# Kernel optimization log

Measured on AMD Instinct MI355X. Metric: run time of the kernel, lower is better.

## Reference

```python
import jax, jax.numpy as jnp
import numpy as np
from jax import lax
from jax.scipy.special import logsumexp

NUM_BINS = 1001          # num_bins
K = 127                  # num_quantized_bins = 2**(8-1) - 1 (signed int8, non-narrow)
HALF = NUM_BINS // 2     # 500
EPS = 1e-4               # smoothing_eps
NEG = -1e30              # mask value for logsumexp


def setup_inputs() -> dict:
    key = jax.random.key(0)
    x = jax.random.normal(key, (8, 4096, 1024), dtype=jnp.float32)
    return {"x": x}


def _smooth_logits(v, valid, L):
    # Faithful to smooth_normalize_distribution: hist += eps*is_zeros - eps1*n_nonzeros
    is_zero = valid & (v == 0)
    n_zeros = jnp.sum(is_zero).astype(jnp.float32)
    n_nz = L.astype(jnp.float32) - n_zeros
    eps1 = EPS * n_zeros / jnp.maximum(n_nz, 1.0)
    logits = v + EPS * is_zero.astype(jnp.float32) - eps1 * n_nz
    return logits, n_nz


def reference(x):
    absmax = jnp.max(jnp.abs(x))
    edges = jnp.linspace(-absmax, absmax, NUM_BINS + 1)           # hist_edges, len 1002
    counts, _ = jnp.histogram(x.ravel(), bins=edges)
    hist = lax.stop_gradient(counts.astype(jnp.float32))          # torch.histc(...).int()
    csum = jnp.concatenate([jnp.zeros(1, jnp.float32), jnp.cumsum(hist)])  # exclusive prefix
    total = csum[-1]
    hist_pad = jnp.concatenate([hist, jnp.zeros(NUM_BINS, jnp.float32)])
    k = jnp.arange(NUM_BINS)

    def per_candidate(i):
        start = HALF - i
        stop = HALF + i + 1
        L = 2 * i + 1                          # length of sliced histogram
        valid = k < L
        sliced = lax.dynamic_slice(hist_pad, (start,), (NUM_BINS,))  # first L entries valid
        left = csum[start]                     # sum(hist[:start])
        right = total - csum[stop]             # sum(hist[stop:])
        p = sliced.at[0].add(left).at[L - 1].add(right)
        m = L // K                             # num_merged_bins
        seg = jnp.minimum(k // m, K - 1)       # merged-bin id per position (remainder -> last)
        seg_v = jnp.where(valid, seg, K)       # dump invalid into extra segment
        qb = jax.ops.segment_sum(jnp.where(valid, sliced, 0.0), seg_v, num_segments=K + 1)[:K]
        nz = valid & (sliced != 0)
        # norm for bin j counts nonzeros in its range; last bin uses stop=-1 (excludes k=L-1)
        cnt_mask = nz & (k != L - 1)
        norms = jax.ops.segment_sum(cnt_mask.astype(jnp.float32), seg_v, num_segments=K + 1)[:K]
        nk = norms[seg]
        qbk = qb[seg]
        # q[start:stop] = qb[j]/norm where norm != 0; k=L-1 never assigned; q[sliced==0]=0
        q = jnp.where(nz & (k != L - 1) & (nk > 0), qbk / jnp.maximum(nk, 1.0), 0.0)

        p_log, _ = _smooth_logits(p, valid, L)
        q_log, n_nz_q = _smooth_logits(q, valid, L)
        lZp = logsumexp(jnp.where(valid, p_log, NEG))
        lZq = logsumexp(jnp.where(valid, q_log, NEG))
        lp = p_log - lZp
        lq = q_log - lZq
        probs = jnp.where(valid, jnp.exp(lp), 0.0)
        kl = jnp.sum(probs * (lp - lq) * valid)
        kl = jnp.where(n_nz_q > 0, kl, jnp.inf)  # q all-zero -> divergence = inf
        return edges[stop], kl

    ivals = jnp.arange(K // 2, HALF + 1)        # i = 63 .. 500 (438 candidates)
    thresholds, divergence = jax.vmap(per_candidate)(ivals)
    return thresholds[jnp.argmin(divergence)]
```

## Files before the change

kernel.cpp:

```cpp
#include <hip/hip_runtime.h>
#include <math.h>

#define NBINS 1001
#define KQ 127
#define HALFB 500
#define SEPS 1e-4f
#define NCAND 438
#define IMIN 63


static __device__ __forceinline__ float edge_at(int j, float stepv, float negabs) {
    return __fadd_rn(__fmul_rn((float)j, stepv), negabs);
}

static __device__ __forceinline__ void blockSum2(double& a, double& b, double* s8) {
    for (int s = 32; s > 0; s >>= 1) {
        a += __shfl_down(a, s, 64);
        b += __shfl_down(b, s, 64);
    }
    const int w = threadIdx.x >> 6, l = threadIdx.x & 63;
    __syncthreads();
    if (l == 0) { s8[w] = a; s8[4 + w] = b; }
    __syncthreads();
    a = (s8[0] + s8[1]) + (s8[2] + s8[3]);
    b = (s8[4] + s8[5]) + (s8[6] + s8[7]);
}

static __device__ __forceinline__ double blockSum1(double a, double* s8) {
    for (int s = 32; s > 0; s >>= 1) a += __shfl_down(a, s, 64);
    const int w = threadIdx.x >> 6, l = threadIdx.x & 63;
    __syncthreads();
    if (l == 0) s8[w] = a;
    __syncthreads();
    return (s8[0] + s8[1]) + (s8[2] + s8[3]);
}

static __device__ __forceinline__ void blockMax2(float& a, float& b, double* s8) {
    for (int s = 32; s > 0; s >>= 1) {
        a = fmaxf(a, __shfl_down(a, s, 64));
        b = fmaxf(b, __shfl_down(b, s, 64));
    }
    const int w = threadIdx.x >> 6, l = threadIdx.x & 63;
    __syncthreads();
    if (l == 0) { s8[w] = (double)a; s8[4 + w] = (double)b; }
    __syncthreads();
    a = fmaxf(fmaxf((float)s8[0], (float)s8[1]), fmaxf((float)s8[2], (float)s8[3]));
    b = fmaxf(fmaxf((float)s8[4], (float)s8[5]), fmaxf((float)s8[6], (float)s8[7]));
}


__global__ void init_kernel(unsigned int* ws_u) {
    int t = threadIdx.x;
    if (t == 0) ws_u[0] = 0u;
    if (t < NBINS) ws_u[4 + t] = 0u;
}

__global__ __launch_bounds__(256) void absmax_kernel(const float* __restrict__ x,
                                                     long long n,
                                                     unsigned int* absmax_bits) {
    __shared__ float red[256];
    float m = 0.f;
    long long idx = (long long)blockIdx.x * blockDim.x + threadIdx.x;
    long long stride = (long long)gridDim.x * blockDim.x;
    const float4* x4 = (const float4*)x;
    long long n4 = n >> 2;
    long long i = idx;
    for (; i + stride < n4; i += 2 * stride) {
        float4 a = x4[i];
        float4 b = x4[i + stride];
        m = fmaxf(m, fmaxf(fmaxf(fabsf(a.x), fabsf(a.y)), fmaxf(fabsf(a.z), fabsf(a.w))));
        m = fmaxf(m, fmaxf(fmaxf(fabsf(b.x), fabsf(b.y)), fmaxf(fabsf(b.z), fabsf(b.w))));
    }
    for (; i < n4; i += stride) {
        float4 a = x4[i];
        m = fmaxf(m, fmaxf(fmaxf(fabsf(a.x), fabsf(a.y)), fmaxf(fabsf(a.z), fabsf(a.w))));
    }
    for (long long j = (n4 << 2) + idx; j < n; j += stride)
        m = fmaxf(m, fabsf(x[j]));
    red[threadIdx.x] = m;
    __syncthreads();
    for (int s = 128; s > 0; s >>= 1) {
        if (threadIdx.x < s) red[threadIdx.x] = fmaxf(red[threadIdx.x], red[threadIdx.x + s]);
        __syncthreads();
    }
    if (threadIdx.x == 0) atomicMax(absmax_bits, __float_as_uint(red[0]));
}

static __device__ __forceinline__ void bin_one(float v, float inv, float cofs,
                                               float stepv, float negabs,
                                               unsigned int* __restrict__ sh) {
    float t = __builtin_fmaf(v, inv, cofs);
    int b = (int)t;
    b = b < 0 ? 0 : (b > NBINS - 1 ? NBINS - 1 : b);
    float e_lo = edge_at(b, stepv, negabs);
    float e_hi = edge_at(b + 1, stepv, negabs);
    int up = (v >= e_hi) & (b < NBINS - 1);
    int dn = (v < e_lo) & (b > 0);
    b += up - dn;
    atomicAdd(&sh[b], 1u);
}

__global__ __launch_bounds__(256) void hist_kernel(const float* __restrict__ x,
                                                   long long n,
                                                   const unsigned int* __restrict__ absmax_bits,
                                                   unsigned int* __restrict__ hist) {
    __shared__ unsigned int sh[4 * NBINS];
    for (int i = threadIdx.x; i < 4 * NBINS; i += blockDim.x) sh[i] = 0u;
    __syncthreads();
    unsigned int* mysh = sh + (threadIdx.x >> 6) * NBINS;

    float absmax = __uint_as_float(*absmax_bits);
    float negabs = -absmax;
    float stepv = __fdiv_rn(__fmul_rn(2.0f, absmax), 1001.0f);
    float inv = __fdiv_rn(1001.0f, __fmul_rn(2.0f, absmax));
    float cofs = __fmul_rn(absmax, inv);

    long long idx = (long long)blockIdx.x * blockDim.x + threadIdx.x;
    long long stride = (long long)gridDim.x * blockDim.x;
    const float4* x4 = (const float4*)x;
    long long n4 = n >> 2;
    long long i = idx;
    for (; i + stride < n4; i += 2 * stride) {
        float4 a = x4[i];
        float4 b = x4[i + stride];
        bin_one(a.x, inv, cofs, stepv, negabs, mysh);
        bin_one(a.y, inv, cofs, stepv, negabs, mysh);
        bin_one(a.z, inv, cofs, stepv, negabs, mysh);
        bin_one(a.w, inv, cofs, stepv, negabs, mysh);
        bin_one(b.x, inv, cofs, stepv, negabs, mysh);
        bin_one(b.y, inv, cofs, stepv, negabs, mysh);
        bin_one(b.z, inv, cofs, stepv, negabs, mysh);
        bin_one(b.w, inv, cofs, stepv, negabs, mysh);
    }
    for (; i < n4; i += stride) {
        float4 a = x4[i];
        bin_one(a.x, inv, cofs, stepv, negabs, mysh);
        bin_one(a.y, inv, cofs, stepv, negabs, mysh);
        bin_one(a.z, inv, cofs, stepv, negabs, mysh);
        bin_one(a.w, inv, cofs, stepv, negabs, mysh);
    }
    for (long long j = (n4 << 2) + idx; j < n; j += stride)
        bin_one(x[j], inv, cofs, stepv, negabs, mysh);

    __syncthreads();
    for (int i2 = threadIdx.x; i2 < NBINS; i2 += blockDim.x) {
        unsigned int s = sh[i2] + sh[NBINS + i2] + sh[2 * NBINS + i2] + sh[3 * NBINS + i2];
        if (s) atomicAdd(&hist[i2], s);
    }
}

__global__ __launch_bounds__(1024) void scan_kernel(const unsigned int* __restrict__ hist,
                                                    double* __restrict__ csumD,
                                                    int* __restrict__ nzc) {
    __shared__ double sd[1024];
    __shared__ int si[1024];
    int t = threadIdx.x;
    unsigned int h = (t < NBINS) ? hist[t] : 0u;
    sd[t] = (double)((float)h);
    si[t] = (t < NBINS && h != 0u) ? 1 : 0;
    __syncthreads();
    for (int off = 1; off < 1024; off <<= 1) {
        double dv = 0.0; int iv = 0;
        if (t >= off) { dv = sd[t - off]; iv = si[t - off]; }
        __syncthreads();
        sd[t] += dv; si[t] += iv;
        __syncthreads();
    }
    if (t < NBINS) { csumD[t + 1] = sd[t]; nzc[t + 1] = si[t]; }
    if (t == 0) { csumD[0] = 0.0; nzc[0] = 0; }
}

__global__ __launch_bounds__(256) void cand_kernel(const unsigned int* __restrict__ hist,
                                                   const double* __restrict__ csumD,
                                                   const int* __restrict__ nzc,
                                                   float* __restrict__ divg) {
    const int i = IMIN + (int)blockIdx.x;
    const int L = 2 * i + 1;
    const int start = HALFB - i;
    const int stop = start + L;
    const int m = L / KQ;
    const unsigned int magic = (65536u + (unsigned)m - 1u) / (unsigned)m;
    const int tid = threadIdx.x;

    __shared__ float s_h[NBINS];
    __shared__ float s_qb[KQ];
    __shared__ float s_nkf[KQ];
    __shared__ double s8[8];

    for (int k = tid; k < NBINS; k += 256) s_h[k] = (float)hist[k];

    double csS = csumD[start], csE = csumD[stop], total = csumD[NBINS];
    float left = (float)csS;
    float right = (float)(total - csE);
    float s0 = (float)hist[start];
    float sL1 = (float)hist[stop - 1];
    int nzwin = nzc[stop] - nzc[start];
    int nnzq = nzwin - ((sL1 != 0.f) ? 1 : 0);
    int nzeros_s = L - nzwin;
    float n_zeros_p = (float)(nzeros_s
                              - ((s0 == 0.f && csS > 0.0) ? 1 : 0)
                              - ((sL1 == 0.f && (total - csE) > 0.0) ? 1 : 0));

    float n_nz_p = (float)L - n_zeros_p;
    float eps1p = SEPS * n_zeros_p / fmaxf(n_nz_p, 1.0f);
    float cp = eps1p * n_nz_p;

    float n_zeros_q = (float)L - (float)nnzq;
    float n_nz_qf = (float)L - n_zeros_q;
    float eps1q = SEPS * n_zeros_q / fmaxf(n_nz_qf, 1.0f);
    float cq = eps1q * n_nz_qf;

    if (tid < KQ) {
        int lo = start + tid * m;
        int hi = (tid == KQ - 1) ? stop : (lo + m);
        s_qb[tid] = (float)(csumD[hi] - csumD[lo]);
        int nrm = (nzc[hi] - nzc[lo]) - ((tid == KQ - 1 && sL1 != 0.f) ? 1 : 0);
        s_nkf[tid] = (float)nrm;
    }
    __syncthreads();

    float ppre[4], qpre[4];
    float maxpp = -INFINITY, maxqq = -INFINITY;
#pragma unroll
    for (int j = 0; j < 4; ++j) {
        int k = tid + 256 * j;
        ppre[j] = 0.f; qpre[j] = 0.f;
        if (k < L) {
            float s = s_h[start + k];
            float p = s;
            if (k == 0) p += left;
            if (k == L - 1) p += right;
            float pp = (p == 0.f) ? SEPS : p;
            int seg = (int)(((unsigned)k * magic) >> 16);
            if (seg > KQ - 1) seg = KQ - 1;
            float qv = 0.f;
            if (s != 0.f && k != L - 1) {
                float nk = s_nkf[seg];
                if (nk > 0.f) qv = s_qb[seg] / nk;
            }
            float qq = (qv == 0.f) ? SEPS : qv;
            ppre[j] = pp; qpre[j] = qq;
            maxpp = fmaxf(maxpp, pp);
            maxqq = fmaxf(maxqq, qq);
        }
    }
    blockMax2(maxpp, maxqq, s8);
    float maxplog = maxpp - cp;
    float maxqlog = maxqq - cq;

    double sp = 0.0, sq = 0.0;
#pragma unroll
    for (int j = 0; j < 4; ++j) {
        int k = tid + 256 * j;
        if (k < L) {
            sp += (double)expf((ppre[j] - cp) - maxplog);
            sq += (double)expf((qpre[j] - cq) - maxqlog);
        }
    }
    blockSum2(sp, sq, s8);
    float lZp = maxplog + (float)log(sp);
    float lZq = maxqlog + (float)log(sq);

    double kll = 0.0;
#pragma unroll
    for (int j = 0; j < 4; ++j) {
        int k = tid + 256 * j;
        if (k < L) {
            float pl = ppre[j] - cp;
            float ql = qpre[j] - cq;
            float lp = pl - lZp;
            float lq = ql - lZq;
            kll += (double)(expf(lp) * (lp - lq));
        }
    }
    double KL = blockSum1(kll, s8);
    if (tid == 0) divg[blockIdx.x] = (nnzq > 0) ? (float)KL : INFINITY;
}

__global__ void argmin_kernel(const float* __restrict__ divg,
                              const unsigned int* __restrict__ absmax_bits,
                              float* __restrict__ out) {
    __shared__ float vals[512];
    __shared__ int idxs[512];
    int tid = threadIdx.x;
    vals[tid] = (tid < NCAND) ? divg[tid] : INFINITY;
    idxs[tid] = tid;
    __syncthreads();
    for (int s = 256; s > 0; s >>= 1) {
        if (tid < s) {
            float a = vals[tid], b = vals[tid + s];
            int ia = idxs[tid], ib = idxs[tid + s];
            if (b < a || (b == a && ib < ia)) { vals[tid] = b; idxs[tid] = ib; }
        }
        __syncthreads();
    }
    if (tid == 0) {
        int i = IMIN + idxs[0];
        int stop = HALFB + i + 1;
        float absmax = __uint_as_float(*absmax_bits);
        float stepv = __fdiv_rn(__fmul_rn(2.0f, absmax), 1001.0f);
        out[0] = __fadd_rn(__fmul_rn((float)stop, stepv), -absmax);
    }
}

extern "C" void kernel_launch(void* const* d_in, const int* in_sizes, int n_in,
                              void* d_out, int out_size, void* d_ws, size_t ws_size,
                              hipStream_t stream) {
    const float* x = (const float*)d_in[0];
    long long n = (long long)in_sizes[0];

    unsigned int* ws_u = (unsigned int*)d_ws;
    unsigned int* absmax_bits = ws_u;
    unsigned int* hist = ws_u + 4;
    float* divg = (float*)(ws_u + 1028);
    double* csumD = (double*)(ws_u + 1536);
    int* nzc = (int*)(ws_u + 3544);
    float* out = (float*)d_out;

    hipLaunchKernelGGL(init_kernel, dim3(1), dim3(1024), 0, stream, ws_u);
    hipLaunchKernelGGL(absmax_kernel, dim3(2048), dim3(256), 0, stream, x, n, absmax_bits);
    hipLaunchKernelGGL(hist_kernel, dim3(1024), dim3(256), 0, stream, x, n, absmax_bits, hist);
    hipLaunchKernelGGL(scan_kernel, dim3(1), dim3(1024), 0, stream, hist, csumD, nzc);
    hipLaunchKernelGGL(cand_kernel, dim3(NCAND), dim3(256), 0, stream, hist, csumD, nzc, divg);
    hipLaunchKernelGGL(argmin_kernel, dim3(1), dim3(512), 0, stream, divg, absmax_bits, out);
}
```

Baseline: 256.5 us.

## Fold init and scan kernels into neighbors, replace absmax atomic with per-block partials

Removes the init kernel by zeroing the histogram in block 0 of the absmax kernel. Absmax now writes per-block partial maxima, which every hist block reduces itself, so the global atomicMax goes away. The single-block scan kernel is removed and each candidate block recomputes the prefix sums in shared memory. The hist grid also doubles to 2048 blocks. This cuts two launches and their serialization, at the cost of redundant scan work in each of 438 blocks and a reduction over 2048 partials in every hist block.

```diff
diff --git a/kernel.cpp b/kernel.cpp
--- a/kernel.cpp
+++ b/kernel.cpp
@@ -7,6 +7,7 @@
 #define SEPS 1e-4f
 #define NCAND 438
 #define IMIN 63
+#define PMAXN 2048
 
 
 static __device__ __forceinline__ float edge_at(int j, float stepv, float negabs) {
@@ -49,16 +50,15 @@
 }
 
 
-__global__ void init_kernel(unsigned int* ws_u) {
-    int t = threadIdx.x;
-    if (t == 0) ws_u[0] = 0u;
-    if (t < NBINS) ws_u[4 + t] = 0u;
-}
-
 __global__ __launch_bounds__(256) void absmax_kernel(const float* __restrict__ x,
                                                      long long n,
-                                                     unsigned int* absmax_bits) {
+                                                     float* __restrict__ pmax,
+                                                     unsigned int* __restrict__ ws_u) {
     __shared__ float red[256];
+    if (blockIdx.x == 0) {
+        for (int t = threadIdx.x; t < NBINS; t += 256) ws_u[4 + t] = 0u;
+        if (threadIdx.x == 0) ws_u[0] = 0u;
+    }
     float m = 0.f;
     long long idx = (long long)blockIdx.x * blockDim.x + threadIdx.x;
     long long stride = (long long)gridDim.x * blockDim.x;
@@ -83,7 +83,7 @@
         if (threadIdx.x < s) red[threadIdx.x] = fmaxf(red[threadIdx.x], red[threadIdx.x + s]);
         __syncthreads();
     }
-    if (threadIdx.x == 0) atomicMax(absmax_bits, __float_as_uint(red[0]));
+    if (threadIdx.x == 0) pmax[blockIdx.x] = red[0];
 }
 
 static __device__ __forceinline__ void bin_one(float v, float inv, float cofs,
@@ -102,14 +102,28 @@
 
 __global__ __launch_bounds__(256) void hist_kernel(const float* __restrict__ x,
                                                    long long n,
-                                                   const unsigned int* __restrict__ absmax_bits,
-                                                   unsigned int* __restrict__ hist) {
+                                                   const float* __restrict__ pmax,
+                                                   unsigned int* __restrict__ hist,
+                                                   unsigned int* __restrict__ absmax_bits) {
     __shared__ unsigned int sh[4 * NBINS];
+    __shared__ float redm[256];
+    {
+        float m = 0.f;
+        for (int t = threadIdx.x; t < PMAXN; t += 256) m = fmaxf(m, pmax[t]);
+        redm[threadIdx.x] = m;
+        __syncthreads();
+        for (int s = 128; s > 0; s >>= 1) {
+            if (threadIdx.x < s) redm[threadIdx.x] = fmaxf(redm[threadIdx.x], redm[threadIdx.x + s]);
+            __syncthreads();
+        }
+    }
+    float absmax = redm[0];
+    if (blockIdx.x == 0 && threadIdx.x == 0) *absmax_bits = __float_as_uint(absmax);
+
     for (int i = threadIdx.x; i < 4 * NBINS; i += blockDim.x) sh[i] = 0u;
     __syncthreads();
     unsigned int* mysh = sh + (threadIdx.x >> 6) * NBINS;
 
-    float absmax = __uint_as_float(*absmax_bits);
     float negabs = -absmax;
     float stepv = __fdiv_rn(__fmul_rn(2.0f, absmax), 1001.0f);
     float inv = __fdiv_rn(1001.0f, __fmul_rn(2.0f, absmax));
@@ -149,30 +163,7 @@
     }
 }
 
-__global__ __launch_bounds__(1024) void scan_kernel(const unsigned int* __restrict__ hist,
-                                                    double* __restrict__ csumD,
-                                                    int* __restrict__ nzc) {
-    __shared__ double sd[1024];
-    __shared__ int si[1024];
-    int t = threadIdx.x;
-    unsigned int h = (t < NBINS) ? hist[t] : 0u;
-    sd[t] = (double)((float)h);
-    si[t] = (t < NBINS && h != 0u) ? 1 : 0;
-    __syncthreads();
-    for (int off = 1; off < 1024; off <<= 1) {
-        double dv = 0.0; int iv = 0;
-        if (t >= off) { dv = sd[t - off]; iv = si[t - off]; }
-        __syncthreads();
-        sd[t] += dv; si[t] += iv;
-        __syncthreads();
-    }
-    if (t < NBINS) { csumD[t + 1] = sd[t]; nzc[t + 1] = si[t]; }
-    if (t == 0) { csumD[0] = 0.0; nzc[0] = 0; }
-}
-
 __global__ __launch_bounds__(256) void cand_kernel(const unsigned int* __restrict__ hist,
-                                                   const double* __restrict__ csumD,
-                                                   const int* __restrict__ nzc,
                                                    float* __restrict__ divg) {
     const int i = IMIN + (int)blockIdx.x;
     const int L = 2 * i + 1;
@@ -183,18 +174,48 @@
     const int tid = threadIdx.x;
 
     __shared__ float s_h[NBINS];
+    __shared__ double sd[1024];
+    __shared__ int si[1024];
     __shared__ float s_qb[KQ];
     __shared__ float s_nkf[KQ];
     __shared__ double s8[8];
 
-    for (int k = tid; k < NBINS; k += 256) s_h[k] = (float)hist[k];
-
-    double csS = csumD[start], csE = csumD[stop], total = csumD[NBINS];
+#pragma unroll
+    for (int j = 0; j < 4; ++j) {
+        int k = tid + 256 * j;
+        unsigned int h = (k < NBINS) ? hist[k] : 0u;
+        float hf = (float)h;
+        if (k < NBINS) s_h[k] = hf;
+        sd[k] = (double)hf;
+        si[k] = (k < NBINS && h != 0u) ? 1 : 0;
+    }
+    __syncthreads();
+
+    for (int off = 1; off < 1024; off <<= 1) {
+        double dv[4]; int iv[4];
+#pragma unroll
+        for (int j = 0; j < 4; ++j) {
+            int k = tid + 256 * j;
+            dv[j] = (k >= off) ? sd[k - off] : 0.0;
+            iv[j] = (k >= off) ? si[k - off] : 0;
+        }
+        __syncthreads();
+#pragma unroll
+        for (int j = 0; j < 4; ++j) {
+            int k = tid + 256 * j;
+            sd[k] += dv[j]; si[k] += iv[j];
+        }
+        __syncthreads();
+    }
+#define CSUM(idx) ((idx) == 0 ? 0.0 : sd[(idx) - 1])
+#define NZC(idx)  ((idx) == 0 ? 0   : si[(idx) - 1])
+
+    double csS = CSUM(start), csE = CSUM(stop), total = CSUM(NBINS);
     float left = (float)csS;
     float right = (float)(total - csE);
-    float s0 = (float)hist[start];
-    float sL1 = (float)hist[stop - 1];
-    int nzwin = nzc[stop] - nzc[start];
+    float s0 = s_h[start];
+    float sL1 = s_h[stop - 1];
+    int nzwin = NZC(stop) - NZC(start);
     int nnzq = nzwin - ((sL1 != 0.f) ? 1 : 0);
     int nzeros_s = L - nzwin;
     float n_zeros_p = (float)(nzeros_s
@@ -213,8 +234,8 @@
     if (tid < KQ) {
         int lo = start + tid * m;
         int hi = (tid == KQ - 1) ? stop : (lo + m);
-        s_qb[tid] = (float)(csumD[hi] - csumD[lo]);
-        int nrm = (nzc[hi] - nzc[lo]) - ((tid == KQ - 1 && sL1 != 0.f) ? 1 : 0);
+        s_qb[tid] = (float)(CSUM(hi) - CSUM(lo));
+        int nrm = (NZC(hi) - NZC(lo)) - ((tid == KQ - 1 && sL1 != 0.f) ? 1 : 0);
         s_nkf[tid] = (float)nrm;
     }
     __syncthreads();
@@ -275,6 +296,8 @@
     }
     double KL = blockSum1(kll, s8);
     if (tid == 0) divg[blockIdx.x] = (nnzq > 0) ? (float)KL : INFINITY;
+#undef CSUM
+#undef NZC
 }
 
 __global__ void argmin_kernel(const float* __restrict__ divg,
@@ -313,14 +336,11 @@
     unsigned int* absmax_bits = ws_u;
     unsigned int* hist = ws_u + 4;
     float* divg = (float*)(ws_u + 1028);
-    double* csumD = (double*)(ws_u + 1536);
-    int* nzc = (int*)(ws_u + 3544);
+    float* pmax = (float*)(ws_u + 2048);
     float* out = (float*)d_out;
 
-    hipLaunchKernelGGL(init_kernel, dim3(1), dim3(1024), 0, stream, ws_u);
-    hipLaunchKernelGGL(absmax_kernel, dim3(2048), dim3(256), 0, stream, x, n, absmax_bits);
-    hipLaunchKernelGGL(hist_kernel, dim3(1024), dim3(256), 0, stream, x, n, absmax_bits, hist);
-    hipLaunchKernelGGL(scan_kernel, dim3(1), dim3(1024), 0, stream, hist, csumD, nzc);
-    hipLaunchKernelGGL(cand_kernel, dim3(NCAND), dim3(256), 0, stream, hist, csumD, nzc, divg);
+    hipLaunchKernelGGL(absmax_kernel, dim3(PMAXN), dim3(256), 0, stream, x, n, pmax, ws_u);
+    hipLaunchKernelGGL(hist_kernel, dim3(2048), dim3(256), 0, stream, x, n, pmax, hist, absmax_bits);
+    hipLaunchKernelGGL(cand_kernel, dim3(NCAND), dim3(256), 0, stream, hist, divg);
     hipLaunchKernelGGL(argmin_kernel, dim3(1), dim3(512), 0, stream, divg, absmax_bits, out);
 }
```

Result: slower. 274.7 us (+7.1%).

## Drop init kernel, use per-block absmax partials, inline ds_add for histogram

Applied to the files above, without the earlier changes.

Removes the separate init kernel by zeroing the workspace inside block 0 of the absmax kernel. Replaces the global atomicMax with per-block partial maxima, which every histogram block re-reduces from 2048 values before binning. Also swaps the LDS atomicAdd for inline ds_add_u32 assembly with an explicit lgkmcnt wait. This saves a launch and a global atomic, at the cost of redundant reduction work per hist block and fragile inline asm.

```diff
diff --git a/kernel.cpp b/kernel.cpp
--- a/kernel.cpp
+++ b/kernel.cpp
@@ -7,6 +7,7 @@
 #define SEPS 1e-4f
 #define NCAND 438
 #define IMIN 63
+#define PMAXN 2048
 
 
 static __device__ __forceinline__ float edge_at(int j, float stepv, float negabs) {
@@ -49,16 +50,15 @@
 }
 
 
-__global__ void init_kernel(unsigned int* ws_u) {
-    int t = threadIdx.x;
-    if (t == 0) ws_u[0] = 0u;
-    if (t < NBINS) ws_u[4 + t] = 0u;
-}
-
 __global__ __launch_bounds__(256) void absmax_kernel(const float* __restrict__ x,
                                                      long long n,
-                                                     unsigned int* absmax_bits) {
+                                                     float* __restrict__ pmax,
+                                                     unsigned int* __restrict__ ws_u) {
     __shared__ float red[256];
+    if (blockIdx.x == 0) {
+        for (int t = threadIdx.x; t < NBINS; t += 256) ws_u[4 + t] = 0u;
+        if (threadIdx.x == 0) ws_u[0] = 0u;
+    }
     float m = 0.f;
     long long idx = (long long)blockIdx.x * blockDim.x + threadIdx.x;
     long long stride = (long long)gridDim.x * blockDim.x;
@@ -83,7 +83,7 @@
         if (threadIdx.x < s) red[threadIdx.x] = fmaxf(red[threadIdx.x], red[threadIdx.x + s]);
         __syncthreads();
     }
-    if (threadIdx.x == 0) atomicMax(absmax_bits, __float_as_uint(red[0]));
+    if (threadIdx.x == 0) pmax[blockIdx.x] = red[0];
 }
 
 static __device__ __forceinline__ void bin_one(float v, float inv, float cofs,
@@ -97,19 +97,34 @@
     int up = (v >= e_hi) & (b < NBINS - 1);
     int dn = (v < e_lo) & (b > 0);
     b += up - dn;
-    atomicAdd(&sh[b], 1u);
+    unsigned int addr = (unsigned int)(unsigned long long)(&sh[b]);
+    asm volatile("ds_add_u32 %0, %1" :: "v"(addr), "v"(1u));
 }
 
 __global__ __launch_bounds__(256) void hist_kernel(const float* __restrict__ x,
                                                    long long n,
-                                                   const unsigned int* __restrict__ absmax_bits,
-                                                   unsigned int* __restrict__ hist) {
+                                                   const float* __restrict__ pmax,
+                                                   unsigned int* __restrict__ hist,
+                                                   unsigned int* __restrict__ absmax_bits) {
     __shared__ unsigned int sh[4 * NBINS];
+    __shared__ float redm[256];
+    {
+        float m = 0.f;
+        for (int t = threadIdx.x; t < PMAXN; t += 256) m = fmaxf(m, pmax[t]);
+        redm[threadIdx.x] = m;
+        __syncthreads();
+        for (int s = 128; s > 0; s >>= 1) {
+            if (threadIdx.x < s) redm[threadIdx.x] = fmaxf(redm[threadIdx.x], redm[threadIdx.x + s]);
+            __syncthreads();
+        }
+    }
+    float absmax = redm[0];
+    if (blockIdx.x == 0 && threadIdx.x == 0) *absmax_bits = __float_as_uint(absmax);
+
     for (int i = threadIdx.x; i < 4 * NBINS; i += blockDim.x) sh[i] = 0u;
     __syncthreads();
     unsigned int* mysh = sh + (threadIdx.x >> 6) * NBINS;
 
-    float absmax = __uint_as_float(*absmax_bits);
     float negabs = -absmax;
     float stepv = __fdiv_rn(__fmul_rn(2.0f, absmax), 1001.0f);
     float inv = __fdiv_rn(1001.0f, __fmul_rn(2.0f, absmax));
@@ -142,6 +157,7 @@
     for (long long j = (n4 << 2) + idx; j < n; j += stride)
         bin_one(x[j], inv, cofs, stepv, negabs, mysh);
 
+    asm volatile("s_waitcnt lgkmcnt(0)" ::: "memory");
     __syncthreads();
     for (int i2 = threadIdx.x; i2 < NBINS; i2 += blockDim.x) {
         unsigned int s = sh[i2] + sh[NBINS + i2] + sh[2 * NBINS + i2] + sh[3 * NBINS + i2];
@@ -315,11 +331,11 @@
     float* divg = (float*)(ws_u + 1028);
     double* csumD = (double*)(ws_u + 1536);
     int* nzc = (int*)(ws_u + 3544);
+    float* pmax = (float*)(ws_u + 4608);
     float* out = (float*)d_out;
 
-    hipLaunchKernelGGL(init_kernel, dim3(1), dim3(1024), 0, stream, ws_u);
-    hipLaunchKernelGGL(absmax_kernel, dim3(2048), dim3(256), 0, stream, x, n, absmax_bits);
-    hipLaunchKernelGGL(hist_kernel, dim3(1024), dim3(256), 0, stream, x, n, absmax_bits, hist);
+    hipLaunchKernelGGL(absmax_kernel, dim3(PMAXN), dim3(256), 0, stream, x, n, pmax, ws_u);
+    hipLaunchKernelGGL(hist_kernel, dim3(1024), dim3(256), 0, stream, x, n, pmax, hist, absmax_bits);
     hipLaunchKernelGGL(scan_kernel, dim3(1), dim3(1024), 0, stream, hist, csumD, nzc);
     hipLaunchKernelGGL(cand_kernel, dim3(NCAND), dim3(256), 0, stream, hist, csumD, nzc, divg);
     hipLaunchKernelGGL(argmin_kernel, dim3(1), dim3(512), 0, stream, divg, absmax_bits, out);
```

After: 245.6 us. -4.2%, faster.
